# Kernel tuning notes

Measured on AMD Instinct MI355X. Metric: run time of the kernel, lower is better.

## Reference

```python
import jax, jax.numpy as jnp
import numpy as np

N_NODES = 50000
N_EDGES = 1600000
IN_CH = 128
OUT_CH = 64
N_HEADS = 4


def setup_inputs() -> dict:
    key = jax.random.key(0)
    k1, k2, k3, k4, k5 = jax.random.split(key, 5)
    x_source = jax.random.normal(k1, (N_NODES, IN_CH), dtype=jnp.float32)
    edge_tgt = jax.random.randint(k2, (N_EDGES,), 0, N_NODES, dtype=jnp.int32)
    edge_src = jax.random.randint(k3, (N_EDGES,), 0, N_NODES, dtype=jnp.int32)
    edge_vals = jnp.ones((N_EDGES,), dtype=jnp.float32)
    # per-head learned params (xavier_uniform-ish scale)
    w_scale = float(np.sqrt(6.0 / (IN_CH + OUT_CH)))
    weight = jax.random.uniform(k4, (N_HEADS, IN_CH, OUT_CH), dtype=jnp.float32,
                                minval=-w_scale, maxval=w_scale)
    a_scale = float(np.sqrt(6.0 / (2 * OUT_CH)))
    att_weight = jax.random.uniform(k5, (N_HEADS, 2 * OUT_CH), dtype=jnp.float32,
                                    minval=-a_scale, maxval=a_scale)
    return {"x_source": x_source, "edge_tgt": edge_tgt, "edge_src": edge_src,
            "edge_vals": edge_vals, "weight": weight, "att_weight": att_weight}


def _can_forward(x_source, edge_tgt, edge_src, edge_vals, weight, att_weight):
    n_nodes = x_source.shape[0]
    out_ch = weight.shape[-1]
    # per-head linear transform: [N, H, O]
    x_msg = jnp.einsum('ni,hio->nho', x_source, weight)
    # gather per-edge source/target messages: [E, H, O]
    src_msg = x_msg[edge_src]
    tgt_msg = x_msg[edge_tgt]
    # attention score = cat([src, tgt]) @ att_weight, split halves: [E, H]
    aw_s = att_weight[:, :out_ch]
    aw_t = att_weight[:, out_ch:]
    e = jnp.einsum('eho,ho->eh', src_msg, aw_s) + jnp.einsum('eho,ho->eh', tgt_msg, aw_t)
    e = jax.nn.leaky_relu(e, negative_slope=0.01)  # default torch slope
    e = e * edge_vals[:, None]  # multiply by neighborhood values pre-softmax
    # sparse softmax over each target row (dim=1 of the sparse matrix)
    row_max = jax.ops.segment_max(e, edge_tgt, num_segments=n_nodes)  # [N, H]
    e_exp = jnp.exp(e - row_max[edge_tgt])
    row_sum = jax.ops.segment_sum(e_exp, edge_tgt, num_segments=n_nodes)  # [N, H]
    alpha = e_exp / row_sum[edge_tgt]  # [E, H]
    # weighted aggregate of source messages per target node: [N, H, O]
    out = jax.ops.segment_sum(alpha[:, :, None] * src_msg, edge_tgt,
                              num_segments=n_nodes)
    # concat heads -> [N, H*O]
    return out.reshape(n_nodes, -1)


def reference(x_source, edge_tgt, edge_src, edge_vals, weight, att_weight):
    return _can_forward(x_source, edge_tgt, edge_src, edge_vals, weight, att_weight)
```

## Files before the change

kernel.cpp:

```cpp
#include <hip/hip_runtime.h>
#include <hip/hip_bf16.h>
#include <math.h>

#define N_NODES 50000
#define N_EDGES 1600000
#define IN_CH   128
#define OUT_CH  64
#define N_HEADS 4
#define CH      (N_HEADS * OUT_CH)

#define NPB   64
#define BINS  782
#define CAPB  3072
#define CHUNK 8000
#define NSCAT 200
#define GEMMB 782

typedef __attribute__((ext_vector_type(8))) short bf16x8;
typedef __attribute__((ext_vector_type(4))) float f32x4;

__device__ __forceinline__ float bf16_lo(unsigned u) { return __uint_as_float(u << 16); }
__device__ __forceinline__ float bf16_hi(unsigned u) { return __uint_as_float(u & 0xffff0000u); }
__device__ __forceinline__ unsigned short f_to_bf16(float f) {
  unsigned u = __float_as_uint(f);
  u += 0x7fffu + ((u >> 16) & 1u);
  return (unsigned short)(u >> 16);
}

__global__ __launch_bounds__(256) void convert_w_init(
    const float* __restrict__ w, unsigned short* __restrict__ wb, int* __restrict__ gcur)
{
  int i = blockIdx.x * 256 + threadIdx.x;
  if (i < BINS) gcur[i] = i * CAPB;
  if (i >= N_HEADS * IN_CH * OUT_CH) return;
  int j = i & 7, lane = (i >> 3) & 63, ctg = (i >> 9) & 15, kc = i >> 13;
  int k = kc * 32 + (lane >> 4) * 8 + j;
  int n = ctg * 16 + (lane & 15);
  int h = n >> 6, o = n & 63;
  wb[i] = f_to_bf16(w[(h * IN_CH + k) * OUT_CH + o]);
}

__global__ __launch_bounds__(256) void gemm_scatter(
    const float* __restrict__ x, const unsigned short* __restrict__ wb,
    const float* __restrict__ aw,
    unsigned short* __restrict__ xmsg, float* __restrict__ sbuf, float* __restrict__ tbuf,
    const int* __restrict__ etgt, const int* __restrict__ esrc,
    const float* __restrict__ eval, int* __restrict__ gcur, int2* __restrict__ binned)
{
  __shared__ __align__(16) char smem[32768];

  if (blockIdx.x < NSCAT) {
    int* lhist = (int*)smem;
    int* lbase = lhist + BINS;
    unsigned short* stg = (unsigned short*)(lbase + BINS);

    const int tid = threadIdx.x;
    const int e0 = blockIdx.x * CHUNK;
    const int n = min(CHUNK, N_EDGES - e0);

    for (int b = tid; b < BINS; b += 256) lhist[b] = 0;
    __syncthreads();

    for (int i = tid; i < n; i += 256) {
      int t = etgt[e0 + i];
      stg[i] = (unsigned short)t;
      atomicAdd(&lhist[t >> 6], 1);
    }
    __syncthreads();

    for (int b = tid; b < BINS; b += 256) {
      int c = lhist[b];
      lbase[b] = c ? atomicAdd(&gcur[b], c) : 0;
      lhist[b] = 0;
    }
    __syncthreads();

    for (int i = tid; i < n; i += 256) {
      int t = (int)stg[i];
      int b = t >> 6;
      int r = atomicAdd(&lhist[b], 1);
      int pos = lbase[b] + r;
      if (pos < (b + 1) * CAPB) {
        int pack = esrc[e0 + i] | ((t & 63) << 16);
        binned[pos] = make_int2(pack, __float_as_int(eval[e0 + i]));
      }
    }
    return;
  }

  unsigned short (*tlds)[32][128] = (unsigned short (*)[32][128])smem;

  const int gbid = blockIdx.x - NSCAT;
  const int lane = threadIdx.x & 63;
  const int wv   = threadIdx.x >> 6;
  const int q    = lane >> 4;
  const int l16  = lane & 15;
  const int rowbase = gbid * 64 + (wv >> 1) * 32;
  const int chalf   = wv & 1;

  bf16x8 afrag[2][4];
  #pragma unroll
  for (int s = 0; s < 2; ++s) {
    int r = rowbase + s * 16 + l16;
    r = min(r, N_NODES - 1);
    const float* xp = x + (size_t)r * IN_CH + q * 8;
    #pragma unroll
    for (int kc = 0; kc < 4; ++kc) {
      f32x4 lo = *(const f32x4*)(xp + kc * 32);
      f32x4 hi = *(const f32x4*)(xp + kc * 32 + 4);
      bf16x8 a;
      a[0] = (short)f_to_bf16(lo[0]); a[1] = (short)f_to_bf16(lo[1]);
      a[2] = (short)f_to_bf16(lo[2]); a[3] = (short)f_to_bf16(lo[3]);
      a[4] = (short)f_to_bf16(hi[0]); a[5] = (short)f_to_bf16(hi[1]);
      a[6] = (short)f_to_bf16(hi[2]); a[7] = (short)f_to_bf16(hi[3]);
      afrag[s][kc] = a;
    }
  }

  f32x4 acc[2][8];
  #pragma unroll
  for (int s = 0; s < 2; ++s)
    #pragma unroll
    for (int ct = 0; ct < 8; ++ct)
      acc[s][ct] = (f32x4){0.f, 0.f, 0.f, 0.f};

  #pragma unroll
  for (int kc = 0; kc < 4; ++kc) {
    #pragma unroll
    for (int ct = 0; ct < 8; ++ct) {
      const int ctg = chalf * 8 + ct;
      bf16x8 b = *(const bf16x8*)(wb + ((size_t)(kc * 16 + ctg) * 64 + lane) * 8);
      acc[0][ct] = __builtin_amdgcn_mfma_f32_16x16x32_bf16(afrag[0][kc], b, acc[0][ct], 0, 0, 0);
      acc[1][ct] = __builtin_amdgcn_mfma_f32_16x16x32_bf16(afrag[1][kc], b, acc[1][ct], 0, 0, 0);
    }
  }

  #pragma unroll
  for (int s = 0; s < 2; ++s)
    #pragma unroll
    for (int ct = 0; ct < 8; ++ct)
      #pragma unroll
      for (int reg = 0; reg < 4; ++reg)
        tlds[wv][s * 16 + q * 4 + reg][ct * 16 + l16] = f_to_bf16(acc[s][ct][reg]);

  #pragma unroll
  for (int s = 0; s < 2; ++s) {
    float ps[2][4] = {{0,0,0,0},{0,0,0,0}};
    float pt[2][4] = {{0,0,0,0},{0,0,0,0}};
    #pragma unroll
    for (int ct = 0; ct < 8; ++ct) {
      int col = chalf * 128 + ct * 16 + l16;
      int h = col >> 6;
      float as_ = aw[h * 128 + (col & 63)];
      float at_ = aw[h * 128 + 64 + (col & 63)];
      int hp = ct >> 2;
      #pragma unroll
      for (int reg = 0; reg < 4; ++reg) {
        float v = acc[s][ct][reg];
        ps[hp][reg] += v * as_;
        pt[hp][reg] += v * at_;
      }
    }
    #pragma unroll
    for (int hp = 0; hp < 2; ++hp)
      #pragma unroll
      for (int reg = 0; reg < 4; ++reg)
        #pragma unroll
        for (int off = 1; off < 16; off <<= 1) {
          ps[hp][reg] += __shfl_xor(ps[hp][reg], off);
          pt[hp][reg] += __shfl_xor(pt[hp][reg], off);
        }
    const int rowq = rowbase + s * 16 + q * 4;
    if (l16 == 0) {
      #pragma unroll
      for (int reg = 0; reg < 4; ++reg) {
        int r = rowq + reg;
        if (r < N_NODES) {
          #pragma unroll
          for (int hp = 0; hp < 2; ++hp) {
            sbuf[r * 4 + chalf * 2 + hp] = ps[hp][reg];
            tbuf[r * 4 + chalf * 2 + hp] = pt[hp][reg];
          }
        }
      }
    }
  }

  __syncthreads();

  const int seg  = lane & 31;
  const int half = lane >> 5;
  #pragma unroll
  for (int r2 = 0; r2 < 16; ++r2) {
    int row = r2 * 2 + half;
    int gr = rowbase + row;
    if (gr < N_NODES) {
      ushort4 vv = *(const ushort4*)&tlds[wv][row][seg * 4];
      *(ushort4*)(xmsg + (size_t)gr * CH + chalf * 128 + seg * 4) = vv;
    }
  }
}

__global__ __launch_bounds__(512, 2) void bin_aggregate(
    const int* __restrict__ gcur, const int2* __restrict__ binned,
    const float* __restrict__ sbuf, const float* __restrict__ tbuf,
    const unsigned short* __restrict__ xmsg, float* __restrict__ out)
{
  __shared__ int nh[NPB];
  __shared__ int start_l[NPB];
  __shared__ int deg_l[NPB];
  __shared__ __align__(16) int2 sorted[CAPB];
  __shared__ int s_lds[8][64];
  __shared__ __align__(16) float p_lds[8][64][4];

  const int tid = threadIdx.x;
  const int b = blockIdx.x;
  const int bbase = b * CAPB;
  const int cnt = min(gcur[b] - bbase, CAPB);

  if (tid < NPB) nh[tid] = 0;
  __syncthreads();

  for (int i = tid; i < cnt; i += 512)
    atomicAdd(&nh[(binned[bbase + i].x >> 16) & 63], 1);
  __syncthreads();

  if (tid < 64) {
    int v = nh[tid];
    int sc = v;
    #pragma unroll
    for (int off = 1; off < 64; off <<= 1) {
      int u = __shfl_up(sc, off);
      if (tid >= off) sc += u;
    }
    start_l[tid] = sc - v;
    deg_l[tid] = v;
    nh[tid] = 0;
  }
  __syncthreads();

  for (int i = tid; i < cnt; i += 512) {
    int2 e = binned[bbase + i];
    int tl = (e.x >> 16) & 63;
    int r = atomicAdd(&nh[tl], 1);
    sorted[start_l[tl] + r] = e;
  }
  __syncthreads();

  const int lane = tid & 63;
  const int wave = tid >> 6;
  const int seg  = lane & 31;
  const int half = lane >> 5;
  const int hh4  = seg >> 3;

  for (int ni = wave * 8; ni < wave * 8 + 8; ++ni) {
    const int n = b * NPB + ni;
    if (n >= N_NODES) break;

    const int d   = deg_l[ni];
    const int rs0 = start_l[ni];

    float4 tn4 = *(const float4*)(tbuf + (size_t)n * 4);
    float tn[4] = {tn4.x, tn4.y, tn4.z, tn4.w};

    float m[4]    = {-INFINITY, -INFINITY, -INFINITY, -INFINITY};
    float psum[4] = {0.f, 0.f, 0.f, 0.f};
    float acc[8]  = {0.f, 0.f, 0.f, 0.f, 0.f, 0.f, 0.f, 0.f};

    for (int base2 = 0; base2 < d; base2 += 64) {
      const int cnt2 = min(64, d - base2);
      const bool act = lane < cnt2;

      float sc4[4] = {-INFINITY, -INFINITY, -INFINITY, -INFINITY};
      int s = 0;
      if (act) {
        int2 ev = sorted[rs0 + base2 + lane];
        s = ev.x & 0xffff;
        float v = __int_as_float(ev.y);
        float4 sv4 = *(const float4*)(sbuf + (size_t)s * 4);
        float svv[4] = {sv4.x, sv4.y, sv4.z, sv4.w};
        #pragma unroll
        for (int hh = 0; hh < 4; ++hh) {
          float t = svv[hh] + tn[hh];
          t = (t > 0.f) ? t : 0.01f * t;
          sc4[hh] = t * v;
        }
      }

      float bm[4] = {sc4[0], sc4[1], sc4[2], sc4[3]};
      #pragma unroll
      for (int hh = 0; hh < 4; ++hh)
        #pragma unroll
        for (int off = 32; off; off >>= 1)
          bm[hh] = fmaxf(bm[hh], __shfl_xor(bm[hh], off));

      float p[4];
      #pragma unroll
      for (int hh = 0; hh < 4; ++hh) {
        float nm = fmaxf(m[hh], bm[hh]);
        float r = (m[hh] == -INFINITY) ? 0.f : __expf(m[hh] - nm);
        psum[hh] *= r;
        if (hh == hh4) {
          #pragma unroll
          for (int j = 0; j < 8; ++j) acc[j] *= r;
        }
        m[hh] = nm;
        p[hh] = act ? __expf(sc4[hh] - nm) : 0.f;
        psum[hh] += p[hh];
      }

      if (act) {
        s_lds[wave][lane] = s;
        *(float4*)(&p_lds[wave][lane][0]) = make_float4(p[0], p[1], p[2], p[3]);
      }
      __builtin_amdgcn_wave_barrier();

      int k = 0;
      for (; k + 8 <= cnt2; k += 8) {
        int sA = s_lds[wave][k + 0 + half];
        int sB = s_lds[wave][k + 2 + half];
        int sC = s_lds[wave][k + 4 + half];
        int sD = s_lds[wave][k + 6 + half];
        uint4 rA = *(const uint4*)(xmsg + (size_t)sA * CH + seg * 8);
        uint4 rB = *(const uint4*)(xmsg + (size_t)sB * CH + seg * 8);
        uint4 rC = *(const uint4*)(xmsg + (size_t)sC * CH + seg * 8);
        uint4 rD = *(const uint4*)(xmsg + (size_t)sD * CH + seg * 8);
        float qA = p_lds[wave][k + 0 + half][hh4];
        float qB = p_lds[wave][k + 2 + half][hh4];
        float qC = p_lds[wave][k + 4 + half][hh4];
        float qD = p_lds[wave][k + 6 + half][hh4];
        acc[0] = fmaf(qA, bf16_lo(rA.x), acc[0]); acc[1] = fmaf(qA, bf16_hi(rA.x), acc[1]);
        acc[2] = fmaf(qA, bf16_lo(rA.y), acc[2]); acc[3] = fmaf(qA, bf16_hi(rA.y), acc[3]);
        acc[4] = fmaf(qA, bf16_lo(rA.z), acc[4]); acc[5] = fmaf(qA, bf16_hi(rA.z), acc[5]);
        acc[6] = fmaf(qA, bf16_lo(rA.w), acc[6]); acc[7] = fmaf(qA, bf16_hi(rA.w), acc[7]);
        acc[0] = fmaf(qB, bf16_lo(rB.x), acc[0]); acc[1] = fmaf(qB, bf16_hi(rB.x), acc[1]);
        acc[2] = fmaf(qB, bf16_lo(rB.y), acc[2]); acc[3] = fmaf(qB, bf16_hi(rB.y), acc[3]);
        acc[4] = fmaf(qB, bf16_lo(rB.z), acc[4]); acc[5] = fmaf(qB, bf16_hi(rB.z), acc[5]);
        acc[6] = fmaf(qB, bf16_lo(rB.w), acc[6]); acc[7] = fmaf(qB, bf16_hi(rB.w), acc[7]);
        acc[0] = fmaf(qC, bf16_lo(rC.x), acc[0]); acc[1] = fmaf(qC, bf16_hi(rC.x), acc[1]);
        acc[2] = fmaf(qC, bf16_lo(rC.y), acc[2]); acc[3] = fmaf(qC, bf16_hi(rC.y), acc[3]);
        acc[4] = fmaf(qC, bf16_lo(rC.z), acc[4]); acc[5] = fmaf(qC, bf16_hi(rC.z), acc[5]);
        acc[6] = fmaf(qC, bf16_lo(rC.w), acc[6]); acc[7] = fmaf(qC, bf16_hi(rC.w), acc[7]);
        acc[0] = fmaf(qD, bf16_lo(rD.x), acc[0]); acc[1] = fmaf(qD, bf16_hi(rD.x), acc[1]);
        acc[2] = fmaf(qD, bf16_lo(rD.y), acc[2]); acc[3] = fmaf(qD, bf16_hi(rD.y), acc[3]);
        acc[4] = fmaf(qD, bf16_lo(rD.z), acc[4]); acc[5] = fmaf(qD, bf16_hi(rD.z), acc[5]);
        acc[6] = fmaf(qD, bf16_lo(rD.w), acc[6]); acc[7] = fmaf(qD, bf16_hi(rD.w), acc[7]);
      }
      for (; k < cnt2; k += 2) {
        int e = k + half;
        if (e < cnt2) {
          int sA = s_lds[wave][e];
          uint4 rA = *(const uint4*)(xmsg + (size_t)sA * CH + seg * 8);
          float qA = p_lds[wave][e][hh4];
          acc[0] = fmaf(qA, bf16_lo(rA.x), acc[0]); acc[1] = fmaf(qA, bf16_hi(rA.x), acc[1]);
          acc[2] = fmaf(qA, bf16_lo(rA.y), acc[2]); acc[3] = fmaf(qA, bf16_hi(rA.y), acc[3]);
          acc[4] = fmaf(qA, bf16_lo(rA.z), acc[4]); acc[5] = fmaf(qA, bf16_hi(rA.z), acc[5]);
          acc[6] = fmaf(qA, bf16_lo(rA.w), acc[6]); acc[7] = fmaf(qA, bf16_hi(rA.w), acc[7]);
        }
      }
      __builtin_amdgcn_wave_barrier();
    }

    #pragma unroll
    for (int j = 0; j < 8; ++j) acc[j] += __shfl_xor(acc[j], 32);
    #pragma unroll
    for (int hh = 0; hh < 4; ++hh)
      #pragma unroll
      for (int off = 32; off; off >>= 1)
        psum[hh] += __shfl_xor(psum[hh], off);

    float rsum = psum[hh4];
    float inv = (rsum > 0.f) ? 1.0f / rsum : 0.f;
    const int o = half * 4;
    float4 o4 = make_float4(acc[o+0]*inv, acc[o+1]*inv, acc[o+2]*inv, acc[o+3]*inv);
    *(float4*)(out + (size_t)n * CH + seg * 8 + half * 4) = o4;
  }
}

extern "C" void kernel_launch(void* const* d_in, const int* in_sizes, int n_in,
                              void* d_out, int out_size, void* d_ws, size_t ws_size,
                              hipStream_t stream) {
  const float* x    = (const float*)d_in[0];
  const int*   etgt = (const int*)  d_in[1];
  const int*   esrc = (const int*)  d_in[2];
  const float* evl  = (const float*)d_in[3];
  const float* w    = (const float*)d_in[4];
  const float* aw   = (const float*)d_in[5];
  float* out = (float*)d_out;

  char* ws = (char*)d_ws;
  unsigned short* wb   = (unsigned short*)(ws);
  unsigned short* xmsg = (unsigned short*)(ws + 65536);
  float* sbuf     = (float*)(ws + 25665536);
  float* tbuf     = (float*)(ws + 26465536);
  int*   gcur     = (int*)  (ws + 27265536);
  int2*  binned   = (int2*) (ws + 27269632);

  convert_w_init<<<128, 256, 0, stream>>>(w, wb, gcur);
  gemm_scatter<<<NSCAT + GEMMB, 256, 0, stream>>>(x, wb, aw, xmsg, sbuf, tbuf,
                                                  etgt, esrc, evl, gcur, binned);
  bin_aggregate<<<BINS, 512, 0, stream>>>(gcur, binned, sbuf, tbuf, xmsg, out);
}
```

Before: 277.8 us.

## Locally sort edges by bin in LDS before coalesced global scatter

The edge-binning phase now builds a per-block prefix sum over bin histograms and counting-sorts each chunk's edges into LDS. It then writes them to the global binned array in sorted order, so consecutive threads write mostly contiguous addresses instead of scattered ones. Chunk size shrinks and the number of scatter blocks grows so the int2 staging buffer fits in shared memory. This adds an extra pass over the edge arrays, an extra LDS round trip and a single-wave scan. The packed word now carries the full target index rather than only its low 6 bits.

```diff
diff --git a/kernel.cpp b/kernel.cpp
--- a/kernel.cpp
+++ b/kernel.cpp
@@ -12,8 +12,8 @@
 #define NPB   64
 #define BINS  782
 #define CAPB  3072
-#define CHUNK 8000
-#define NSCAT 200
+#define CHUNK 2560
+#define NSCAT 625
 #define GEMMB 782
 
 typedef __attribute__((ext_vector_type(8))) short bf16x8;
@@ -50,9 +50,10 @@
   __shared__ __align__(16) char smem[32768];
 
   if (blockIdx.x < NSCAT) {
-    int* lhist = (int*)smem;
-    int* lbase = lhist + BINS;
-    unsigned short* stg = (unsigned short*)(lbase + BINS);
+    int* lhist  = (int*)smem;
+    int* lstart = lhist + BINS;
+    int* lbase  = lstart + BINS;
+    int2* stg   = (int2*)(lbase + BINS);
 
     const int tid = threadIdx.x;
     const int e0 = blockIdx.x * CHUNK;
@@ -61,10 +62,24 @@
     for (int b = tid; b < BINS; b += 256) lhist[b] = 0;
     __syncthreads();
 
-    for (int i = tid; i < n; i += 256) {
-      int t = etgt[e0 + i];
-      stg[i] = (unsigned short)t;
-      atomicAdd(&lhist[t >> 6], 1);
+    for (int i = tid; i < n; i += 256)
+      atomicAdd(&lhist[etgt[e0 + i] >> 6], 1);
+    __syncthreads();
+
+    if (tid < 64) {
+      int carry = 0;
+      for (int c = 0; c < BINS; c += 64) {
+        int idx = c + tid;
+        int v = (idx < BINS) ? lhist[idx] : 0;
+        int sc = v;
+        #pragma unroll
+        for (int off = 1; off < 64; off <<= 1) {
+          int u = __shfl_up(sc, off);
+          if (tid >= off) sc += u;
+        }
+        if (idx < BINS) lstart[idx] = carry + sc - v;
+        carry += __shfl(sc, 63);
+      }
     }
     __syncthreads();
 
@@ -76,14 +91,20 @@
     __syncthreads();
 
     for (int i = tid; i < n; i += 256) {
-      int t = (int)stg[i];
+      int t = etgt[e0 + i];
       int b = t >> 6;
       int r = atomicAdd(&lhist[b], 1);
-      int pos = lbase[b] + r;
-      if (pos < (b + 1) * CAPB) {
-        int pack = esrc[e0 + i] | ((t & 63) << 16);
-        binned[pos] = make_int2(pack, __float_as_int(eval[e0 + i]));
-      }
+      unsigned pack = (unsigned)esrc[e0 + i] | ((unsigned)t << 16);
+      stg[lstart[b] + r] = make_int2((int)pack, __float_as_int(eval[e0 + i]));
+    }
+    __syncthreads();
+
+    for (int i = tid; i < n; i += 256) {
+      int2 e = stg[i];
+      int b = (int)(((unsigned)e.x) >> 22);
+      int gpos = lbase[b] + (i - lstart[b]);
+      if (gpos < (b + 1) * CAPB)
+        binned[gpos] = e;
     }
     return;
   }
```

After: 278.7 us. No clear change (+0.3%).
